# Kernel tuning notes

Hardware: AMD Instinct MI355X
Metric: run time of the kernel (lower is better)

The kernel has to match this reference:

```python
import jax, jax.numpy as jnp
import numpy as np

D_IN = 1024
D_OUT = 1024
NUM_HEADS = 16
HEAD_DIM = D_OUT // NUM_HEADS


def setup_inputs() -> dict:
    key = jax.random.key(0)
    k = jax.random.split(key, 6)
    s = 1.0 / np.sqrt(D_IN)
    return {
        "x": jax.random.normal(k[0], (2, 2048, D_IN), dtype=jnp.float32),
        "W_q": jax.random.uniform(k[1], (D_OUT, D_IN), jnp.float32, -s, s),
        "W_k": jax.random.uniform(k[2], (D_OUT, D_IN), jnp.float32, -s, s),
        "W_v": jax.random.uniform(k[3], (D_OUT, D_IN), jnp.float32, -s, s),
        "W_o": jax.random.uniform(k[4], (D_OUT, D_OUT), jnp.float32, -s, s),
        "b_o": jax.random.uniform(k[5], (D_OUT,), jnp.float32, -s, s),
    }


def reference(x, W_q, W_k, W_v, W_o, b_o):
    b, n, _ = x.shape
    h, hd = NUM_HEADS, HEAD_DIM
    # linear projections (torch Linear: x @ W.T), reshape to [b, h, n, hd]
    q = (x @ W_q.T).reshape(b, n, h, hd).transpose(0, 2, 1, 3)
    k = (x @ W_k.T).reshape(b, n, h, hd).transpose(0, 2, 1, 3)
    v = (x @ W_v.T).reshape(b, n, h, hd).transpose(0, 2, 1, 3)
    scores = jnp.einsum("bhqd,bhkd->bhqk", q, k) / np.sqrt(hd).astype(np.float32)
    causal = jnp.triu(jnp.full((n, n), -jnp.inf, dtype=scores.dtype), k=1)
    scores = scores + causal[None, None]
    weights = jax.nn.softmax(scores, axis=-1)  # dropout p=0.0 -> identity
    ctx = jnp.einsum("bhqk,bhkd->bhqd", weights, v)
    ctx = ctx.transpose(0, 2, 1, 3).reshape(b, n, h * hd)
    return ctx @ W_o.T + b_o
```

## Files before the change

### kernel.cpp

```cpp
#include <hip/hip_runtime.h>
#include <hip/hip_bf16.h>
#include <stdint.h>

typedef __attribute__((ext_vector_type(8)))  __bf16   bf16x8;
typedef __attribute__((ext_vector_type(4)))  float    f32x4;
typedef __attribute__((ext_vector_type(16))) float    f32x16;
typedef __attribute__((ext_vector_type(4)))  unsigned u32x4;
typedef __attribute__((ext_vector_type(2)))  unsigned u32x2;

#define BATCH  2
#define SEQ    2048
#define DMODEL 1024
#define NHEAD  16
#define HDIM   64
#define MTOT   (BATCH * SEQ)
#define MOFF   8.0f

__device__ __forceinline__ void gload_lds16(const void* g, void* l) {
  __builtin_amdgcn_global_load_lds(
      (const __attribute__((address_space(1))) unsigned int*)g,
      (__attribute__((address_space(3))) unsigned int*)(uintptr_t)l,
      16, 0, 0);
}

__device__ __forceinline__ unsigned pkbf(float a, float b) {
  unsigned lo = (unsigned)__builtin_bit_cast(unsigned short, (__bf16)a);
  unsigned hb = (unsigned)__builtin_bit_cast(unsigned short, (__bf16)b);
  return lo | (hb << 16);
}

__global__ void cast_all(const float* __restrict__ x,  const float* __restrict__ wq,
                         const float* __restrict__ wk, const float* __restrict__ wv,
                         const float* __restrict__ wo,
                         __bf16* __restrict__ xb,  __bf16* __restrict__ wqb,
                         __bf16* __restrict__ wkb, __bf16* __restrict__ wvb,
                         __bf16* __restrict__ wob)
{
  const float* in; __bf16* out; int n;
  switch (blockIdx.y) {
    case 0:  in = x;  out = xb;  n = MTOT * DMODEL;   break;
    case 1:  in = wq; out = wqb; n = DMODEL * DMODEL; break;
    case 2:  in = wk; out = wkb; n = DMODEL * DMODEL; break;
    case 3:  in = wv; out = wvb; n = DMODEL * DMODEL; break;
    default: in = wo; out = wob; n = DMODEL * DMODEL; break;
  }
  const int i = blockIdx.x * blockDim.x + threadIdx.x;
  const int stride = gridDim.x * blockDim.x;
  for (int idx = i; idx * 8 < n; idx += stride) {
    const float4 a = ((const float4*)in)[idx * 2];
    const float4 b = ((const float4*)in)[idx * 2 + 1];
    bf16x8 v = { (__bf16)a.x, (__bf16)a.y, (__bf16)a.z, (__bf16)a.w,
                 (__bf16)b.x, (__bf16)b.y, (__bf16)b.z, (__bf16)b.w };
    *(bf16x8*)(out + (size_t)idx * 8) = v;
  }
}

__device__ __forceinline__ void gemm_tile_128(const __bf16* __restrict__ A,
                                              const __bf16* __restrict__ W,
                                              int bm, int bn, int Kd,
                                              f32x4 (&acc)[4][4])
{
  __shared__ __align__(16) __bf16 As[128 * 32];
  __shared__ __align__(16) __bf16 Bs[128 * 32];
  const int tid  = threadIdx.x;
  const int wave = tid >> 6, lane = tid & 63;
  const int wr = wave >> 1, wc = wave & 1;
  const int fr = lane & 15, fq = lane >> 4;
  const int c0 = tid, c1 = tid + 256;
  const __bf16* gA0 = A + (size_t)(bm * 128 + (c0 >> 2)) * Kd + (c0 & 3) * 8;
  const __bf16* gA1 = A + (size_t)(bm * 128 + (c1 >> 2)) * Kd + (c1 & 3) * 8;
  const __bf16* gB0 = W + (size_t)(bn * 128 + (c0 >> 2)) * Kd + (c0 & 3) * 8;
  const __bf16* gB1 = W + (size_t)(bn * 128 + (c1 >> 2)) * Kd + (c1 & 3) * 8;

  for (int k0 = 0; k0 < Kd; k0 += 32) {
    gload_lds16(gA0 + k0, As + c0 * 8);
    gload_lds16(gB0 + k0, Bs + c0 * 8);
    gload_lds16(gA1 + k0, As + c1 * 8);
    gload_lds16(gB1 + k0, Bs + c1 * 8);
    __syncthreads();
    bf16x8 a[4], b[4];
#pragma unroll
    for (int m = 0; m < 4; ++m)
      a[m] = *(const bf16x8*)(As + (wr * 64 + m * 16 + fr) * 32 + fq * 8);
#pragma unroll
    for (int n = 0; n < 4; ++n)
      b[n] = *(const bf16x8*)(Bs + (wc * 64 + n * 16 + fr) * 32 + fq * 8);
#pragma unroll
    for (int m = 0; m < 4; ++m)
#pragma unroll
      for (int n = 0; n < 4; ++n)
        acc[m][n] = __builtin_amdgcn_mfma_f32_16x16x32_bf16(a[m], b[n], acc[m][n], 0, 0, 0);
    __syncthreads();
  }
}

__global__ __launch_bounds__(256)
void gemm_qkv(const __bf16* __restrict__ xb,
              const __bf16* __restrict__ Wq, const __bf16* __restrict__ Wk,
              const __bf16* __restrict__ Wv,
              __bf16* __restrict__ Qo, __bf16* __restrict__ Ko, __bf16* __restrict__ VTo,
              float qscale)
{
  const int z = blockIdx.z;
  const __bf16* A; const __bf16* W; __bf16* Ob; int bm, bn;
  if (z == 2)      { A = Wv; W = xb; Ob = VTo; bm = blockIdx.y; bn = blockIdx.x; }
  else if (z == 1) { A = xb; W = Wk; Ob = Ko;  bm = blockIdx.x; bn = blockIdx.y; }
  else             { A = xb; W = Wq; Ob = Qo;  bm = blockIdx.x; bn = blockIdx.y; }

  f32x4 acc[4][4] = {};
  gemm_tile_128(A, W, bm, bn, DMODEL, acc);

  const int lane = threadIdx.x & 63, wave = threadIdx.x >> 6;
  const int wr = wave >> 1, wc = wave & 1;
  const int fr = lane & 15, fq = lane >> 4;

  if (z == 0) {
#pragma unroll
    for (int m = 0; m < 4; ++m)
#pragma unroll
      for (int n = 0; n < 4; ++n) {
        const int col = bn * 128 + wc * 64 + n * 16 + fr;
#pragma unroll
        for (int j = 0; j < 4; ++j) {
          const int row = bm * 128 + wr * 64 + m * 16 + fq * 4 + j;
          Ob[(size_t)row * DMODEL + col] = (__bf16)(acc[m][n][j] * qscale);
        }
      }
  } else if (z == 1) {
#pragma unroll
    for (int m = 0; m < 4; ++m)
#pragma unroll
      for (int n = 0; n < 4; ++n) {
        const int f = bn * 128 + wc * 64 + n * 16 + fr;
        const int h = f >> 6;
        const int kc = (f >> 4) & 3, hi = (f >> 3) & 1, jj = f & 7;
#pragma unroll
        for (int j = 0; j < 4; ++j) {
          const int tkn = bm * 128 + wr * 64 + m * 16 + fq * 4 + j;
          const int bb = tkn >> 11, n2 = tkn & 2047;
          const int t32 = n2 >> 5, ln2 = n2 & 31;
          const size_t idx = (((((size_t)bb * 16 + h) * 64 + t32) * 4 + kc) * 64
                              + (ln2 + (hi << 5))) * 8 + jj;
          Ob[idx] = (__bf16)acc[m][n][j];
        }
      }
  } else {
#pragma unroll
    for (int m = 0; m < 4; ++m)
#pragma unroll
      for (int n = 0; n < 4; ++n) {
        const int tkn = bn * 128 + wc * 64 + n * 16 + fr;
        const int bb = tkn >> 11, n2 = tkn & 2047;
        const int t64 = n2 >> 6, w2 = n2 & 63;
        const int kc = w2 >> 4, hi = (w2 >> 3) & 1, jj = w2 & 7;
#pragma unroll
        for (int j = 0; j < 4; ++j) {
          const int f = bm * 128 + wr * 64 + m * 16 + fq * 4 + j;
          const int h = f >> 6, d = f & 63;
          const int db = d >> 5, ln2 = d & 31;
          const size_t idx = ((((((size_t)bb * 16 + h) * 32 + t64) * 2 + db) * 4 + kc) * 64
                              + (ln2 + (hi << 5))) * 8 + jj;
          Ob[idx] = (__bf16)acc[m][n][j];
        }
      }
  }
}

__global__ __launch_bounds__(256)
void gemm_out(const __bf16* __restrict__ A, const __bf16* __restrict__ W,
              float* __restrict__ OF, const float* __restrict__ bias)
{
  f32x4 acc[4][4] = {};
  gemm_tile_128(A, W, blockIdx.x, blockIdx.y, DMODEL, acc);

  const int lane = threadIdx.x & 63, wave = threadIdx.x >> 6;
  const int wr = wave >> 1, wc = wave & 1;
  const int fr = lane & 15, fq = lane >> 4;
#pragma unroll
  for (int m = 0; m < 4; ++m)
#pragma unroll
    for (int n = 0; n < 4; ++n) {
      const int col = blockIdx.y * 128 + wc * 64 + n * 16 + fr;
#pragma unroll
      for (int j = 0; j < 4; ++j) {
        const int row = blockIdx.x * 128 + wr * 64 + m * 16 + fq * 4 + j;
        OF[(size_t)row * DMODEL + col] = acc[m][n][j] + bias[col];
      }
    }
}


__device__ __forceinline__ void mask_tile(f32x16& sv0, f32x16& sv1,
                                          int kv0, int q0, int ln, int hi)
{
  const int qg = q0 + ln;
#pragma unroll
  for (int r = 0; r < 16; ++r) {
    const int kvo = kv0 + (r & 3) + 8 * (r >> 2) + 4 * hi;
    if (kvo > qg)      sv0[r] = -1e30f;
    if (kvo + 32 > qg) sv1[r] = -1e30f;
  }
}

__device__ __forceinline__ void stream_fin(f32x16& sv0, f32x16& sv1, float& l_acc,
                                           f32x16& c0, f32x16& c1,
                                           const bf16x8 (&vt0)[4], const bf16x8 (&vt1)[4],
                                           int hi)
{
#pragma unroll
  for (int r = 0; r < 16; ++r) {
    sv0[r] = __builtin_amdgcn_exp2f(sv0[r] - MOFF);
    sv1[r] = __builtin_amdgcn_exp2f(sv1[r] - MOFF);
  }
  float s8[8];
#pragma unroll
  for (int r = 0; r < 8; ++r)
    s8[r] = (sv0[r] + sv0[r + 8]) + (sv1[r] + sv1[r + 8]);
#pragma unroll
  for (int r = 0; r < 4; ++r) s8[r] += s8[r + 4];
  l_acc += (s8[0] + s8[1]) + (s8[2] + s8[3]);

  bf16x8 pf[4];
#pragma unroll
  for (int half = 0; half < 2; ++half) {
    const int r0 = half * 8;
    {
      unsigned pk01 = pkbf(sv0[r0 + 0], sv0[r0 + 1]);
      unsigned pk23 = pkbf(sv0[r0 + 2], sv0[r0 + 3]);
      unsigned pk45 = pkbf(sv0[r0 + 4], sv0[r0 + 5]);
      unsigned pk67 = pkbf(sv0[r0 + 6], sv0[r0 + 7]);
      unsigned x01 = (unsigned)__shfl_xor((int)pk01, 32, 64);
      unsigned x23 = (unsigned)__shfl_xor((int)pk23, 32, 64);
      unsigned x45 = (unsigned)__shfl_xor((int)pk45, 32, 64);
      unsigned x67 = (unsigned)__shfl_xor((int)pk67, 32, 64);
      u32x4 uw = { hi ? x45 : pk01, hi ? x67 : pk23,
                   hi ? pk45 : x01, hi ? pk67 : x23 };
      pf[half] = __builtin_bit_cast(bf16x8, uw);
    }
    {
      unsigned pk01 = pkbf(sv1[r0 + 0], sv1[r0 + 1]);
      unsigned pk23 = pkbf(sv1[r0 + 2], sv1[r0 + 3]);
      unsigned pk45 = pkbf(sv1[r0 + 4], sv1[r0 + 5]);
      unsigned pk67 = pkbf(sv1[r0 + 6], sv1[r0 + 7]);
      unsigned x01 = (unsigned)__shfl_xor((int)pk01, 32, 64);
      unsigned x23 = (unsigned)__shfl_xor((int)pk23, 32, 64);
      unsigned x45 = (unsigned)__shfl_xor((int)pk45, 32, 64);
      unsigned x67 = (unsigned)__shfl_xor((int)pk67, 32, 64);
      u32x4 uw = { hi ? x45 : pk01, hi ? x67 : pk23,
                   hi ? pk45 : x01, hi ? pk67 : x23 };
      pf[2 + half] = __builtin_bit_cast(bf16x8, uw);
    }
  }

  __builtin_amdgcn_s_setprio(1);
#pragma unroll
  for (int kc = 0; kc < 4; ++kc)
    c0 = __builtin_amdgcn_mfma_f32_32x32x16_bf16(vt0[kc], pf[kc], c0, 0, 0, 0);
#pragma unroll
  for (int kc = 0; kc < 4; ++kc)
    c1 = __builtin_amdgcn_mfma_f32_32x32x16_bf16(vt1[kc], pf[kc], c1, 0, 0, 0);
  __builtin_amdgcn_s_setprio(0);
}

__global__ __launch_bounds__(256)
void attn_kernel(const __bf16* __restrict__ Qg, const __bf16* __restrict__ PK,
                 const __bf16* __restrict__ PV, __bf16* __restrict__ Og)
{
  __shared__ __align__(16) float Cs[4][32][68];
  __shared__ float Ls[4][2][32];

  const int tid  = threadIdx.x;
  const int p    = tid >> 6;
  const int lane = tid & 63;
  const int ln = lane & 31, hi = lane >> 5;
  const int bI = blockIdx.x;
  const int bh = bI & 31;
  const int jp = bI >> 5;
  const int b = bh >> 4, h = bh & 15;

  const int qtL = jp, qtH = 63 - jp;
  const int q0L = qtL * 32, q0H = qtH * 32;
  const int ntL = (qtL >> 1) + 1, ntH = (qtH >> 1) + 1;

  const __bf16* Kp  = PK + (size_t)(b * 16 + h) * (64 * 4 * 64 * 8);
  const __bf16* Vp  = PV + (size_t)(b * 16 + h) * (32 * 2 * 4 * 64 * 8);
  const __bf16* QpL = Qg + ((size_t)b * SEQ + q0L + ln) * DMODEL + h * HDIM + hi * 8;
  const __bf16* QpH = Qg + ((size_t)b * SEQ + q0H + ln) * DMODEL + h * HDIM + hi * 8;

  bf16x8 qfL[4], qfH[4];
#pragma unroll
  for (int kc = 0; kc < 4; ++kc) {
    qfL[kc] = *(const bf16x8*)(QpL + kc * 16);
    qfH[kc] = *(const bf16x8*)(QpH + kc * 16);
  }

  f32x16 cL0 = {}, cL1 = {}, cH0 = {}, cH1 = {};
  float lL = 0.f, lH = 0.f;

  for (int t = p; t < ntH; t += 4) {
    const __bf16* kt = Kp + (size_t)t * 4096;
    const __bf16* vt = Vp + (size_t)t * 4096;

    bf16x8 kA[4], kB[4], vt0[4], vt1[4];
#pragma unroll
    for (int kc = 0; kc < 4; ++kc) {
      kA[kc]  = *(const bf16x8*)(kt + (kc * 64 + lane) * 8);
      kB[kc]  = *(const bf16x8*)(kt + 2048 + (kc * 64 + lane) * 8);
    }
#pragma unroll
    for (int kc = 0; kc < 4; ++kc) {
      vt0[kc] = *(const bf16x8*)(vt + (kc * 64 + lane) * 8);
      vt1[kc] = *(const bf16x8*)(vt + 2048 + (kc * 64 + lane) * 8);
    }

    const int kv0 = t * 64;

    {
      f32x16 s0 = {}, s1 = {};
      __builtin_amdgcn_s_setprio(1);
#pragma unroll
      for (int kc = 0; kc < 4; ++kc) {
        s0 = __builtin_amdgcn_mfma_f32_32x32x16_bf16(kA[kc], qfH[kc], s0, 0, 0, 0);
        s1 = __builtin_amdgcn_mfma_f32_32x32x16_bf16(kB[kc], qfH[kc], s1, 0, 0, 0);
      }
      __builtin_amdgcn_s_setprio(0);
      if (t == ntH - 1) mask_tile(s0, s1, kv0, q0H, ln, hi);
      stream_fin(s0, s1, lH, cH0, cH1, vt0, vt1, hi);
    }

    if (t < ntL) {
      f32x16 s0 = {}, s1 = {};
      __builtin_amdgcn_s_setprio(1);
#pragma unroll
      for (int kc = 0; kc < 4; ++kc) {
        s0 = __builtin_amdgcn_mfma_f32_32x32x16_bf16(kA[kc], qfL[kc], s0, 0, 0, 0);
        s1 = __builtin_amdgcn_mfma_f32_32x32x16_bf16(kB[kc], qfL[kc], s1, 0, 0, 0);
      }
      __builtin_amdgcn_s_setprio(0);
      if (t == ntL - 1) mask_tile(s0, s1, kv0, q0L, ln, hi);
      stream_fin(s0, s1, lL, cL0, cL1, vt0, vt1, hi);
    }
  }

  const int qe = (p << 3) | (lane >> 3);
  const int de = (lane & 7) * 8;

#pragma unroll
  for (int g = 0; g < 4; ++g) {
    f32x4 v0 = { cL0[4*g+0], cL0[4*g+1], cL0[4*g+2], cL0[4*g+3] };
    f32x4 v1 = { cL1[4*g+0], cL1[4*g+1], cL1[4*g+2], cL1[4*g+3] };
    *(f32x4*)&Cs[p][ln][g * 8 + hi * 4]      = v0;
    *(f32x4*)&Cs[p][ln][32 + g * 8 + hi * 4] = v1;
  }
  Ls[p][hi][ln] = lL;
  __syncthreads();

  {
    float lt = 0.f;
#pragma unroll
    for (int pp = 0; pp < 4; ++pp) lt += Ls[pp][0][qe] + Ls[pp][1][qe];
    const float inv = 1.0f / lt;
    f32x4 a0 = {}, a1 = {};
#pragma unroll
    for (int pp = 0; pp < 4; ++pp) {
      a0 += *(const f32x4*)&Cs[pp][qe][de];
      a1 += *(const f32x4*)&Cs[pp][qe][de + 4];
    }
    u32x4 w = { pkbf(a0[0] * inv, a0[1] * inv), pkbf(a0[2] * inv, a0[3] * inv),
                pkbf(a1[0] * inv, a1[1] * inv), pkbf(a1[2] * inv, a1[3] * inv) };
    *(u32x4*)(Og + ((size_t)b * SEQ + q0L + qe) * DMODEL + h * HDIM + de) = w;
  }
  __syncthreads();

#pragma unroll
  for (int g = 0; g < 4; ++g) {
    f32x4 v0 = { cH0[4*g+0], cH0[4*g+1], cH0[4*g+2], cH0[4*g+3] };
    f32x4 v1 = { cH1[4*g+0], cH1[4*g+1], cH1[4*g+2], cH1[4*g+3] };
    *(f32x4*)&Cs[p][ln][g * 8 + hi * 4]      = v0;
    *(f32x4*)&Cs[p][ln][32 + g * 8 + hi * 4] = v1;
  }
  Ls[p][hi][ln] = lH;
  __syncthreads();

  {
    float lt = 0.f;
#pragma unroll
    for (int pp = 0; pp < 4; ++pp) lt += Ls[pp][0][qe] + Ls[pp][1][qe];
    const float inv = 1.0f / lt;
    f32x4 a0 = {}, a1 = {};
#pragma unroll
    for (int pp = 0; pp < 4; ++pp) {
      a0 += *(const f32x4*)&Cs[pp][qe][de];
      a1 += *(const f32x4*)&Cs[pp][qe][de + 4];
    }
    u32x4 w = { pkbf(a0[0] * inv, a0[1] * inv), pkbf(a0[2] * inv, a0[3] * inv),
                pkbf(a1[0] * inv, a1[1] * inv), pkbf(a1[2] * inv, a1[3] * inv) };
    *(u32x4*)(Og + ((size_t)b * SEQ + q0H + qe) * DMODEL + h * HDIM + de) = w;
  }
}

extern "C" void kernel_launch(void* const* d_in, const int* in_sizes, int n_in,
                              void* d_out, int out_size, void* d_ws, size_t ws_size,
                              hipStream_t stream) {
  (void)in_sizes; (void)n_in; (void)out_size; (void)ws_size;
  const float* x  = (const float*)d_in[0];
  const float* Wq = (const float*)d_in[1];
  const float* Wk = (const float*)d_in[2];
  const float* Wv = (const float*)d_in[3];
  const float* Wo = (const float*)d_in[4];
  const float* bo = (const float*)d_in[5];
  float* out = (float*)d_out;

  __bf16* ws  = (__bf16*)d_ws;
  __bf16* xb  = ws;
  __bf16* Wqb = xb  + (size_t)MTOT * DMODEL;
  __bf16* Wkb = Wqb + (size_t)DMODEL * DMODEL;
  __bf16* Wvb = Wkb + (size_t)DMODEL * DMODEL;
  __bf16* Wob = Wvb + (size_t)DMODEL * DMODEL;
  __bf16* Qb  = Wob + (size_t)DMODEL * DMODEL;
  __bf16* Kpk = Qb  + (size_t)MTOT * DMODEL;
  __bf16* Vpk = Kpk + (size_t)MTOT * DMODEL;
  __bf16* ctxb = xb;

  cast_all<<<dim3(256, 5), 256, 0, stream>>>(x, Wq, Wk, Wv, Wo,
                                             xb, Wqb, Wkb, Wvb, Wob);

  const float qscale = 0.125f * 1.4426950408889634f;
  gemm_qkv<<<dim3(32, 8, 3), 256, 0, stream>>>(xb, Wqb, Wkb, Wvb, Qb, Kpk, Vpk, qscale);

  attn_kernel<<<dim3(1024), 256, 0, stream>>>(Qb, Kpk, Vpk, ctxb);

  gemm_out<<<dim3(32, 8), 256, 0, stream>>>(ctxb, Wob, out, bo);
}
```

Baseline: 121.5 us.

## Split attention into one q-tile per block with two waves, heaviest tiles first

The attention kernel no longer pairs a low and a high causal q-tile in one 4-wave block. It launches 2048 blocks of 128 threads, each handling a single 32-row q-tile with two waves splitting the KV tiles, ordered so the longest tiles are scheduled first. V loads are moved after the QK MFMAs to shorten register live ranges, and launch bounds request 3 blocks per CU. This trades the balanced L/H pairing for finer-grained scheduling and lower register pressure, but it doubles the block count and loses K/V reuse across the two q-tiles.

```diff
diff --git a/kernel.cpp b/kernel.cpp
--- a/kernel.cpp
+++ b/kernel.cpp
@@ -202,25 +202,9 @@
   }
 }
 
-__device__ __forceinline__ void stream_fin(f32x16& sv0, f32x16& sv1, float& l_acc,
-                                           f32x16& c0, f32x16& c1,
-                                           const bf16x8 (&vt0)[4], const bf16x8 (&vt1)[4],
-                                           int hi)
-{
-#pragma unroll
-  for (int r = 0; r < 16; ++r) {
-    sv0[r] = __builtin_amdgcn_exp2f(sv0[r] - MOFF);
-    sv1[r] = __builtin_amdgcn_exp2f(sv1[r] - MOFF);
-  }
-  float s8[8];
-#pragma unroll
-  for (int r = 0; r < 8; ++r)
-    s8[r] = (sv0[r] + sv0[r + 8]) + (sv1[r] + sv1[r + 8]);
-#pragma unroll
-  for (int r = 0; r < 4; ++r) s8[r] += s8[r + 4];
-  l_acc += (s8[0] + s8[1]) + (s8[2] + s8[3]);
-
-  bf16x8 pf[4];
+__device__ __forceinline__ void pack_pf(const f32x16& sv0, const f32x16& sv1,
+                                        bf16x8 (&pf)[4], int hi)
+{
 #pragma unroll
   for (int half = 0; half < 2; ++half) {
     const int r0 = half * 8;
@@ -251,23 +235,14 @@
       pf[2 + half] = __builtin_bit_cast(bf16x8, uw);
     }
   }
-
-  __builtin_amdgcn_s_setprio(1);
-#pragma unroll
-  for (int kc = 0; kc < 4; ++kc)
-    c0 = __builtin_amdgcn_mfma_f32_32x32x16_bf16(vt0[kc], pf[kc], c0, 0, 0, 0);
-#pragma unroll
-  for (int kc = 0; kc < 4; ++kc)
-    c1 = __builtin_amdgcn_mfma_f32_32x32x16_bf16(vt1[kc], pf[kc], c1, 0, 0, 0);
-  __builtin_amdgcn_s_setprio(0);
-}
-
-__global__ __launch_bounds__(256)
+}
+
+__global__ __launch_bounds__(128, 3)
 void attn_kernel(const __bf16* __restrict__ Qg, const __bf16* __restrict__ PK,
                  const __bf16* __restrict__ PV, __bf16* __restrict__ Og)
 {
-  __shared__ __align__(16) float Cs[4][32][68];
-  __shared__ float Ls[4][2][32];
+  __shared__ __align__(16) float Cs[2][32][68];
+  __shared__ float Ls[2][2][32];
 
   const int tid  = threadIdx.x;
   const int p    = tid >> 6;
@@ -275,128 +250,104 @@
   const int ln = lane & 31, hi = lane >> 5;
   const int bI = blockIdx.x;
   const int bh = bI & 31;
-  const int jp = bI >> 5;
+  const int qt = 63 - (bI >> 5);
   const int b = bh >> 4, h = bh & 15;
 
-  const int qtL = jp, qtH = 63 - jp;
-  const int q0L = qtL * 32, q0H = qtH * 32;
-  const int ntL = (qtL >> 1) + 1, ntH = (qtH >> 1) + 1;
-
-  const __bf16* Kp  = PK + (size_t)(b * 16 + h) * (64 * 4 * 64 * 8);
-  const __bf16* Vp  = PV + (size_t)(b * 16 + h) * (32 * 2 * 4 * 64 * 8);
-  const __bf16* QpL = Qg + ((size_t)b * SEQ + q0L + ln) * DMODEL + h * HDIM + hi * 8;
-  const __bf16* QpH = Qg + ((size_t)b * SEQ + q0H + ln) * DMODEL + h * HDIM + hi * 8;
-
-  bf16x8 qfL[4], qfH[4];
-#pragma unroll
-  for (int kc = 0; kc < 4; ++kc) {
-    qfL[kc] = *(const bf16x8*)(QpL + kc * 16);
-    qfH[kc] = *(const bf16x8*)(QpH + kc * 16);
-  }
-
-  f32x16 cL0 = {}, cL1 = {}, cH0 = {}, cH1 = {};
-  float lL = 0.f, lH = 0.f;
-
-  for (int t = p; t < ntH; t += 4) {
+  const int q0 = qt * 32;
+  const int nt = (qt >> 1) + 1;
+
+  const __bf16* Kp = PK + (size_t)(b * 16 + h) * (64 * 4 * 64 * 8);
+  const __bf16* Vp = PV + (size_t)(b * 16 + h) * (32 * 2 * 4 * 64 * 8);
+  const __bf16* Qp = Qg + ((size_t)b * SEQ + q0 + ln) * DMODEL + h * HDIM + hi * 8;
+
+  bf16x8 qf[4];
+#pragma unroll
+  for (int kc = 0; kc < 4; ++kc)
+    qf[kc] = *(const bf16x8*)(Qp + kc * 16);
+
+  f32x16 c0 = {}, c1 = {};
+  float l = 0.f;
+
+  for (int t = p; t < nt; t += 2) {
     const __bf16* kt = Kp + (size_t)t * 4096;
     const __bf16* vt = Vp + (size_t)t * 4096;
 
-    bf16x8 kA[4], kB[4], vt0[4], vt1[4];
+    bf16x8 kA[4], kB[4];
 #pragma unroll
     for (int kc = 0; kc < 4; ++kc) {
-      kA[kc]  = *(const bf16x8*)(kt + (kc * 64 + lane) * 8);
-      kB[kc]  = *(const bf16x8*)(kt + 2048 + (kc * 64 + lane) * 8);
-    }
+      kA[kc] = *(const bf16x8*)(kt + (kc * 64 + lane) * 8);
+      kB[kc] = *(const bf16x8*)(kt + 2048 + (kc * 64 + lane) * 8);
+    }
+
+    f32x16 s0 = {}, s1 = {};
+    __builtin_amdgcn_s_setprio(1);
+#pragma unroll
+    for (int kc = 0; kc < 4; ++kc) {
+      s0 = __builtin_amdgcn_mfma_f32_32x32x16_bf16(kA[kc], qf[kc], s0, 0, 0, 0);
+      s1 = __builtin_amdgcn_mfma_f32_32x32x16_bf16(kB[kc], qf[kc], s1, 0, 0, 0);
+    }
+    __builtin_amdgcn_s_setprio(0);
+
+    bf16x8 vt0[4], vt1[4];
 #pragma unroll
     for (int kc = 0; kc < 4; ++kc) {
       vt0[kc] = *(const bf16x8*)(vt + (kc * 64 + lane) * 8);
       vt1[kc] = *(const bf16x8*)(vt + 2048 + (kc * 64 + lane) * 8);
     }
 
-    const int kv0 = t * 64;
-
-    {
-      f32x16 s0 = {}, s1 = {};
-      __builtin_amdgcn_s_setprio(1);
-#pragma unroll
-      for (int kc = 0; kc < 4; ++kc) {
-        s0 = __builtin_amdgcn_mfma_f32_32x32x16_bf16(kA[kc], qfH[kc], s0, 0, 0, 0);
-        s1 = __builtin_amdgcn_mfma_f32_32x32x16_bf16(kB[kc], qfH[kc], s1, 0, 0, 0);
-      }
-      __builtin_amdgcn_s_setprio(0);
-      if (t == ntH - 1) mask_tile(s0, s1, kv0, q0H, ln, hi);
-      stream_fin(s0, s1, lH, cH0, cH1, vt0, vt1, hi);
-    }
-
-    if (t < ntL) {
-      f32x16 s0 = {}, s1 = {};
-      __builtin_amdgcn_s_setprio(1);
-#pragma unroll
-      for (int kc = 0; kc < 4; ++kc) {
-        s0 = __builtin_amdgcn_mfma_f32_32x32x16_bf16(kA[kc], qfL[kc], s0, 0, 0, 0);
-        s1 = __builtin_amdgcn_mfma_f32_32x32x16_bf16(kB[kc], qfL[kc], s1, 0, 0, 0);
-      }
-      __builtin_amdgcn_s_setprio(0);
-      if (t == ntL - 1) mask_tile(s0, s1, kv0, q0L, ln, hi);
-      stream_fin(s0, s1, lL, cL0, cL1, vt0, vt1, hi);
-    }
-  }
-
-  const int qe = (p << 3) | (lane >> 3);
-  const int de = (lane & 7) * 8;
+    if (t == nt - 1) mask_tile(s0, s1, t * 64, q0, ln, hi);
+
+#pragma unroll
+    for (int r = 0; r < 16; ++r) {
+      s0[r] = __builtin_amdgcn_exp2f(s0[r] - MOFF);
+      s1[r] = __builtin_amdgcn_exp2f(s1[r] - MOFF);
+    }
+    float s8[8];
+#pragma unroll
+    for (int r = 0; r < 8; ++r)
+      s8[r] = (s0[r] + s0[r + 8]) + (s1[r] + s1[r + 8]);
+#pragma unroll
+    for (int r = 0; r < 4; ++r) s8[r] += s8[r + 4];
+    l += (s8[0] + s8[1]) + (s8[2] + s8[3]);
+
+    bf16x8 pf[4];
+    pack_pf(s0, s1, pf, hi);
+
+    __builtin_amdgcn_s_setprio(1);
+#pragma unroll
+    for (int kc = 0; kc < 4; ++kc)
+      c0 = __builtin_amdgcn_mfma_f32_32x32x16_bf16(vt0[kc], pf[kc], c0, 0, 0, 0);
+#pragma unroll
+    for (int kc = 0; kc < 4; ++kc)
+      c1 = __builtin_amdgcn_mfma_f32_32x32x16_bf16(vt1[kc], pf[kc], c1, 0, 0, 0);
+    __builtin_amdgcn_s_setprio(0);
+  }
 
 #pragma unroll
   for (int g = 0; g < 4; ++g) {
-    f32x4 v0 = { cL0[4*g+0], cL0[4*g+1], cL0[4*g+2], cL0[4*g+3] };
-    f32x4 v1 = { cL1[4*g+0], cL1[4*g+1], cL1[4*g+2], cL1[4*g+3] };
+    f32x4 v0 = { c0[4*g+0], c0[4*g+1], c0[4*g+2], c0[4*g+3] };
+    f32x4 v1 = { c1[4*g+0], c1[4*g+1], c1[4*g+2], c1[4*g+3] };
     *(f32x4*)&Cs[p][ln][g * 8 + hi * 4]      = v0;
     *(f32x4*)&Cs[p][ln][32 + g * 8 + hi * 4] = v1;
   }
-  Ls[p][hi][ln] = lL;
+  Ls[p][hi][ln] = l;
   __syncthreads();
 
-  {
-    float lt = 0.f;
-#pragma unroll
-    for (int pp = 0; pp < 4; ++pp) lt += Ls[pp][0][qe] + Ls[pp][1][qe];
-    const float inv = 1.0f / lt;
-    f32x4 a0 = {}, a1 = {};
-#pragma unroll
-    for (int pp = 0; pp < 4; ++pp) {
-      a0 += *(const f32x4*)&Cs[pp][qe][de];
-      a1 += *(const f32x4*)&Cs[pp][qe][de + 4];
-    }
-    u32x4 w = { pkbf(a0[0] * inv, a0[1] * inv), pkbf(a0[2] * inv, a0[3] * inv),
-                pkbf(a1[0] * inv, a1[1] * inv), pkbf(a1[2] * inv, a1[3] * inv) };
-    *(u32x4*)(Og + ((size_t)b * SEQ + q0L + qe) * DMODEL + h * HDIM + de) = w;
-  }
-  __syncthreads();
-
-#pragma unroll
-  for (int g = 0; g < 4; ++g) {
-    f32x4 v0 = { cH0[4*g+0], cH0[4*g+1], cH0[4*g+2], cH0[4*g+3] };
-    f32x4 v1 = { cH1[4*g+0], cH1[4*g+1], cH1[4*g+2], cH1[4*g+3] };
-    *(f32x4*)&Cs[p][ln][g * 8 + hi * 4]      = v0;
-    *(f32x4*)&Cs[p][ln][32 + g * 8 + hi * 4] = v1;
-  }
-  Ls[p][hi][ln] = lH;
-  __syncthreads();
-
-  {
-    float lt = 0.f;
-#pragma unroll
-    for (int pp = 0; pp < 4; ++pp) lt += Ls[pp][0][qe] + Ls[pp][1][qe];
-    const float inv = 1.0f / lt;
-    f32x4 a0 = {}, a1 = {};
-#pragma unroll
-    for (int pp = 0; pp < 4; ++pp) {
-      a0 += *(const f32x4*)&Cs[pp][qe][de];
-      a1 += *(const f32x4*)&Cs[pp][qe][de + 4];
-    }
-    u32x4 w = { pkbf(a0[0] * inv, a0[1] * inv), pkbf(a0[2] * inv, a0[3] * inv),
-                pkbf(a1[0] * inv, a1[1] * inv), pkbf(a1[2] * inv, a1[3] * inv) };
-    *(u32x4*)(Og + ((size_t)b * SEQ + q0H + qe) * DMODEL + h * HDIM + de) = w;
-  }
+  const int qe = p * 16 + (lane >> 2);
+  const int de = (lane & 3) * 16;
+  const float lt = Ls[0][0][qe] + Ls[0][1][qe] + Ls[1][0][qe] + Ls[1][1][qe];
+  const float inv = 1.0f / lt;
+  f32x4 a0 = *(const f32x4*)&Cs[0][qe][de]      + *(const f32x4*)&Cs[1][qe][de];
+  f32x4 a1 = *(const f32x4*)&Cs[0][qe][de + 4]  + *(const f32x4*)&Cs[1][qe][de + 4];
+  f32x4 a2 = *(const f32x4*)&Cs[0][qe][de + 8]  + *(const f32x4*)&Cs[1][qe][de + 8];
+  f32x4 a3 = *(const f32x4*)&Cs[0][qe][de + 12] + *(const f32x4*)&Cs[1][qe][de + 12];
+  u32x4 w0 = { pkbf(a0[0] * inv, a0[1] * inv), pkbf(a0[2] * inv, a0[3] * inv),
+               pkbf(a1[0] * inv, a1[1] * inv), pkbf(a1[2] * inv, a1[3] * inv) };
+  u32x4 w1 = { pkbf(a2[0] * inv, a2[1] * inv), pkbf(a2[2] * inv, a2[3] * inv),
+               pkbf(a3[0] * inv, a3[1] * inv), pkbf(a3[2] * inv, a3[3] * inv) };
+  __bf16* Op = Og + ((size_t)b * SEQ + q0 + qe) * DMODEL + h * HDIM + de;
+  *(u32x4*)(Op)     = w0;
+  *(u32x4*)(Op + 8) = w1;
 }
 
 extern "C" void kernel_launch(void* const* d_in, const int* in_sizes, int n_in,
@@ -428,7 +379,7 @@
   const float qscale = 0.125f * 1.4426950408889634f;
   gemm_qkv<<<dim3(32, 8, 3), 256, 0, stream>>>(xb, Wqb, Wkb, Wvb, Qb, Kpk, Vpk, qscale);
 
-  attn_kernel<<<dim3(1024), 256, 0, stream>>>(Qb, Kpk, Vpk, ctxb);
+  attn_kernel<<<dim3(2048), 128, 0, stream>>>(Qb, Kpk, Vpk, ctxb);
 
   gemm_out<<<dim3(32, 8), 256, 0, stream>>>(ctxb, Wob, out, bo);
 }
```

Measured after the change: 100.2 us. -17.5%, faster.
